# Kernel tuning notes

Hardware: AMD Instinct MI355X
Metric: run time of the kernel (lower is better)

Reference implementation:

```python
import jax, jax.numpy as jnp
import numpy as np

HID = 128
N_NODES = 50000
N_EDGES = 640000
N_GRAPHS = 64
N_LAYERS = 3
LN_EPS = 1e-5


def _ln(h, g, b):
    mu = jnp.mean(h, axis=-1, keepdims=True)
    v = jnp.mean(jnp.square(h - mu), axis=-1, keepdims=True)
    return (h - mu) * jax.lax.rsqrt(v + LN_EPS) * g + b


def _mlp2(h, W1, b1, g, be, W2, b2):
    # Linear -> ReLU -> LayerNorm -> (Dropout=identity in eval) -> Linear
    h = _ln(jax.nn.relu(h @ W1.T + b1), g, be)
    return h @ W2.T + b2


def _forward(x, edge_index, batch, axis_W1, axis_b1, axis_g, axis_be, axis_W2, axis_b2, org_W1, org_b1, org_g, org_be, org_W2, org_b2, nin_W, nin_b, conv_W1, conv_b1, conv_g, conv_be, conv_W2, conv_b2, eps, ln_g, ln_b, gate_W1, gate_b1, gate_g, gate_be, gate_W2, gate_b2, head_W1, head_b1, head_g, head_be, head_W2, head_b2):
    axis = x[:, 9:12]
    origin = x[:, 12:15]
    others = jnp.concatenate([x[:, :9], x[:, 15:19]], axis=1)  # [N, 13]
    axis_z = _mlp2(axis, axis_W1, axis_b1, axis_g, axis_be, axis_W2, axis_b2)
    org_z = _mlp2(origin, org_W1, org_b1, org_g, org_be, org_W2, org_b2)
    h = jnp.concatenate([others, axis_z, org_z], axis=1) @ nin_W.T + nin_b  # [N, HID]
    src, dst = edge_index[0], edge_index[1]
    n = x.shape[0]
    for l in range(N_LAYERS):
        res = h
        # GIN: sum-aggregate source features into targets (gather + scatter-add)
        agg = jax.ops.segment_sum(h[src], dst, num_segments=n)
        m = (1.0 + eps[l]) * h + agg
        m = _mlp2(m, conv_W1[l], conv_b1[l], conv_g[l], conv_be[l], conv_W2[l], conv_b2[l])
        h = _ln(jax.nn.relu(m), ln_g[l], ln_b[l]) + res
    # AttentionalAggregation: segment softmax over per-graph node gates
    gate = _mlp2(h, gate_W1, gate_b1, gate_g, gate_be, gate_W2, gate_b2)  # [N, 1]
    gmax = jax.ops.segment_max(gate, batch, num_segments=N_GRAPHS)
    e = jnp.exp(gate - gmax[batch])
    denom = jax.ops.segment_sum(e, batch, num_segments=N_GRAPHS)
    attn = e / denom[batch]
    g = jax.ops.segment_sum(attn * h, batch, num_segments=N_GRAPHS)  # [B, HID]
    logit = _mlp2(g, head_W1, head_b1, head_g, head_be, head_W2, head_b2)[:, 0]
    return logit


def setup_inputs() -> dict:
    key = jax.random.key(0)
    ks = iter(jax.random.split(key, 64))
    nk = lambda: next(ks)
    lin = lambda o, i: jax.random.normal(nk(), (o, i), jnp.float32) / np.float32(np.sqrt(i))
    lin3 = lambda L, o, i: jnp.stack([lin(o, i) for _ in range(L)])
    z = lambda *s: jnp.zeros(s, jnp.float32)
    o = lambda *s: jnp.ones(s, jnp.float32)
    inp = {}
    inp['x'] = jax.random.normal(nk(), (N_NODES, 19), jnp.float32)
    inp['edge_index'] = jax.random.randint(nk(), (2, N_EDGES), 0, N_NODES)
    inp['batch'] = jnp.sort(jax.random.randint(nk(), (N_NODES,), 0, N_GRAPHS))
    for p in ('axis', 'org'):
        inp[p + '_W1'] = lin(16, 3); inp[p + '_b1'] = z(16)
        inp[p + '_g'] = o(16); inp[p + '_be'] = z(16)
        inp[p + '_W2'] = lin(16, 16); inp[p + '_b2'] = z(16)
    inp['nin_W'] = lin(HID, 45); inp['nin_b'] = z(HID)
    inp['conv_W1'] = lin3(N_LAYERS, HID, HID); inp['conv_b1'] = z(N_LAYERS, HID)
    inp['conv_g'] = o(N_LAYERS, HID); inp['conv_be'] = z(N_LAYERS, HID)
    inp['conv_W2'] = lin3(N_LAYERS, HID, HID); inp['conv_b2'] = z(N_LAYERS, HID)
    inp['eps'] = z(N_LAYERS)
    inp['ln_g'] = o(N_LAYERS, HID); inp['ln_b'] = z(N_LAYERS, HID)
    for p in ('gate', 'head'):
        inp[p + '_W1'] = lin(HID // 2, HID); inp[p + '_b1'] = z(HID // 2)
        inp[p + '_g'] = o(HID // 2); inp[p + '_be'] = z(HID // 2)
        inp[p + '_W2'] = lin(1, HID // 2); inp[p + '_b2'] = z(1)
    return inp


def reference(x, edge_index, batch, axis_W1, axis_b1, axis_g, axis_be, axis_W2, axis_b2, org_W1, org_b1, org_g, org_be, org_W2, org_b2, nin_W, nin_b, conv_W1, conv_b1, conv_g, conv_be, conv_W2, conv_b2, eps, ln_g, ln_b, gate_W1, gate_b1, gate_g, gate_be, gate_W2, gate_b2, head_W1, head_b1, head_g, head_be, head_W2, head_b2):
    return _forward(x, edge_index, batch, axis_W1, axis_b1, axis_g, axis_be, axis_W2, axis_b2, org_W1, org_b1, org_g, org_be, org_W2, org_b2, nin_W, nin_b, conv_W1, conv_b1, conv_g, conv_be, conv_W2, conv_b2, eps, ln_g, ln_b, gate_W1, gate_b1, gate_g, gate_be, gate_W2, gate_b2, head_W1, head_b1, head_g, head_be, head_W2, head_b2)
```

## Files before the change

kernel.cpp:

```cpp
#include <hip/hip_runtime.h>

#define N_NODESC 50000
#define N_EDGESC 640000
#define N_GRAPHSC 64
#define HIDC 128
#define LN_EPSF 1e-5f
#define NGRID64 ((N_NODESC + 63) / 64)
#define PREP_ELEMS (8192 + 49152 + 49152)
#define WPREP_NB ((PREP_ELEMS + 255) / 256)
#define B1C 200
#define BCHUNK 3200
#define NBUK 98
#define WBUK 512

typedef short bf16x8 __attribute__((ext_vector_type(8)));
typedef float f32x4 __attribute__((ext_vector_type(4)));

static __device__ __forceinline__ unsigned short f2bf(float x) {
  unsigned u = __float_as_uint(x);
  u += 0x7fffu + ((u >> 16) & 1u);
  return (unsigned short)(u >> 16);
}
static __device__ __forceinline__ float bf2f(unsigned short b) {
  return __uint_as_float(((unsigned)b) << 16);
}

static __device__ __forceinline__ void mlp16(float in0, float in1, float in2,
    const float* __restrict__ W1, const float* __restrict__ b1,
    const float* __restrict__ g, const float* __restrict__ be,
    const float* __restrict__ W2, const float* __restrict__ b2,
    float* __restrict__ out) {
  float h[16];
  float s1 = 0.f, s2 = 0.f;
#pragma unroll
  for (int j = 0; j < 16; ++j) {
    float v = b1[j] + W1[j*3+0]*in0 + W1[j*3+1]*in1 + W1[j*3+2]*in2;
    v = fmaxf(v, 0.f);
    h[j] = v; s1 += v; s2 += v*v;
  }
  float mu = s1 * (1.f/16.f);
  float var = fmaxf(s2 * (1.f/16.f) - mu*mu, 0.f);
  float rs = rsqrtf(var + LN_EPSF);
  float z[16];
#pragma unroll
  for (int j = 0; j < 16; ++j) z[j] = (h[j]-mu)*rs*g[j] + be[j];
#pragma unroll
  for (int j = 0; j < 16; ++j) {
    float v = b2[j];
#pragma unroll
    for (int k = 0; k < 16; ++k) v += W2[j*16+k]*z[k];
    out[j] = v;
  }
}

__global__ __launch_bounds__(256) void bin_count_kernel(const int* __restrict__ ei,
    int* __restrict__ counts,
    float* __restrict__ Szero,
    const float* __restrict__ ninW, unsigned short* __restrict__ ninWb,
    const float* __restrict__ cW1, unsigned short* __restrict__ cW1b,
    const float* __restrict__ cW2, unsigned short* __restrict__ cW2b) {
  const int b = blockIdx.x;
  if (b < B1C) {
    __shared__ int cnt[NBUK];
    for (int i = threadIdx.x; i < NBUK; i += 256) cnt[i] = 0;
    __syncthreads();
    const int e0 = b * BCHUNK;
    const int e1 = e0 + BCHUNK;
    for (int e = e0 + threadIdx.x; e < e1; e += 256)
      atomicAdd(&cnt[ei[N_EDGESC + e] >> 9], 1);
    __syncthreads();
    for (int i = threadIdx.x; i < NBUK; i += 256)
      counts[i * B1C + b] = cnt[i];
  } else if (b == B1C) {
    for (int i = threadIdx.x; i < N_GRAPHSC * HIDC + N_GRAPHSC; i += 256)
      Szero[i] = 0.f;
  } else {
    int i = (b - B1C - 1) * 256 + threadIdx.x;
    if (i < 8192) {
      int f = i >> 6, k = i & 63;
      ninWb[i] = (k < 45) ? f2bf(ninW[f*45 + k]) : (unsigned short)0;
    } else if (i < 8192 + 49152) {
      int j = i - 8192;
      cW1b[j] = f2bf(cW1[j]);
    } else if (i < PREP_ELEMS) {
      int j = i - 8192 - 49152;
      cW2b[j] = f2bf(cW2[j]);
    }
  }
}

// ... 191 lines not shown
    int n = __shfl_up(c, off);
    if (lane >= off) c += n;
  }
  if (lane == 63) wsum[w] = c;
  __syncthreads();
  if (t == 0) {
    int run = 0;
#pragma unroll
    for (int k = 0; k < 4; ++k) { int x = wsum[k]; wsum[k] = run; run += x; }
  }
  __syncthreads();
  const int e1 = tot0 + c + wsum[w] - v1;
  hist[t] = e0;
  hist[256 + t] = e1;
  const int n0 = node0 + t, n1 = node0 + 256 + t;
  if (n0 < N_NODESC) rowptr[n0] = base + e0;
  if (n1 < N_NODESC) rowptr[n1] = base + e1;
  __syncthreads();
  for (int p = base + t; p < end; p += 256) {
    int2 pr = pairs[p];
    int slot = base + atomicAdd(&hist[pr.y - node0], 1);
    esrc[slot] = pr.x;
  }
  if (b == NBUK - 1 && t == 0) rowptr[N_NODESC] = N_EDGESC;
}

__global__ __launch_bounds__(128) void agg_kernel(const unsigned short* __restrict__ Hb,
    const int* __restrict__ rowptr, const int* __restrict__ esrc,
    const float* __restrict__ epsp, unsigned short* __restrict__ Mb) {
  const int t = threadIdx.x;
  const int c8 = t & 15;
  const int v  = t >> 4;
  const int node = blockIdx.x * 8 + v;
  if (node >= N_NODESC) return;
  const float e1 = 1.0f + epsp[0];
  bf16x8 h = *(const bf16x8*)&Hb[node*HIDC + c8*8];
  float acc[8];
#pragma unroll
  for (int k = 0; k < 8; ++k) acc[k] = 0.f;
  int s = rowptr[node];
  const int e = rowptr[node+1];
  for (; s + 8 <= e; s += 8) {
    int i0 = esrc[s],   i1 = esrc[s+1], i2 = esrc[s+2], i3 = esrc[s+3];
    int i4 = esrc[s+4], i5 = esrc[s+5], i6 = esrc[s+6], i7 = esrc[s+7];
    bf16x8 x0 = *(const bf16x8*)&Hb[i0*HIDC + c8*8];
    bf16x8 x1 = *(const bf16x8*)&Hb[i1*HIDC + c8*8];
    bf16x8 x2 = *(const bf16x8*)&Hb[i2*HIDC + c8*8];
    bf16x8 x3 = *(const bf16x8*)&Hb[i3*HIDC + c8*8];
    bf16x8 x4 = *(const bf16x8*)&Hb[i4*HIDC + c8*8];
    bf16x8 x5 = *(const bf16x8*)&Hb[i5*HIDC + c8*8];
    bf16x8 x6 = *(const bf16x8*)&Hb[i6*HIDC + c8*8];
    bf16x8 x7 = *(const bf16x8*)&Hb[i7*HIDC + c8*8];
#pragma unroll
    for (int k = 0; k < 8; ++k)
      acc[k] += ((bf2f((unsigned short)x0[k]) + bf2f((unsigned short)x1[k]))
               + (bf2f((unsigned short)x2[k]) + bf2f((unsigned short)x3[k])))
              + ((bf2f((unsigned short)x4[k]) + bf2f((unsigned short)x5[k]))
               + (bf2f((unsigned short)x6[k]) + bf2f((unsigned short)x7[k])));
  }
  for (; s + 4 <= e; s += 4) {
    int i0 = esrc[s], i1 = esrc[s+1], i2 = esrc[s+2], i3 = esrc[s+3];
    bf16x8 x0 = *(const bf16x8*)&Hb[i0*HIDC + c8*8];
    bf16x8 x1 = *(const bf16x8*)&Hb[i1*HIDC + c8*8];
    bf16x8 x2 = *(const bf16x8*)&Hb[i2*HIDC + c8*8];
    bf16x8 x3 = *(const bf16x8*)&Hb[i3*HIDC + c8*8];
#pragma unroll
    for (int k = 0; k < 8; ++k)
      acc[k] += (bf2f((unsigned short)x0[k]) + bf2f((unsigned short)x1[k]))
              + (bf2f((unsigned short)x2[k]) + bf2f((unsigned short)x3[k]));
  }
  for (; s < e; ++s) {
    bf16x8 x0 = *(const bf16x8*)&Hb[esrc[s]*HIDC + c8*8];
#pragma unroll
    for (int k = 0; k < 8; ++k) acc[k] += bf2f((unsigned short)x0[k]);
  }
  bf16x8 m8;
#pragma unroll
  for (int k = 0; k < 8; ++k)
    m8[k] = (short)f2bf(e1*bf2f((unsigned short)h[k]) + acc[k]);
  *(bf16x8*)&Mb[node*HIDC + c8*8] = m8;
}

template<bool GATE>
__global__ __launch_bounds__(256, 3) void gemmpair_kernel(
    const unsigned short* __restrict__ Mb,
    const unsigned short* __restrict__ Hin,
    const unsigned short* __restrict__ W1b, const float* __restrict__ b1,
    const float* __restrict__ g1, const float* __restrict__ be1,
    const unsigned short* __restrict__ W2b, const float* __restrict__ b2,
    const float* __restrict__ lng, const float* __restrict__ lnb,
    unsigned short* __restrict__ Hout,
    const float* __restrict__ gW1, const float* __restrict__ gb1,
    const float* __restrict__ glng, const float* __restrict__ glnb,
    const float* __restrict__ gW2, const float* __restrict__ gb2,
    const int* __restrict__ batch, float* __restrict__ S,
    float* __restrict__ denom) {
  __shared__ unsigned short Ab[64*136];
  __shared__ unsigned short Wl[128*136];
  __shared__ float Egate[64];
  __shared__ int   Sbatch[64];
  const int t = threadIdx.x;
  const int nb = blockIdx.x * 64;

#pragma unroll
  for (int i = 0; i < 4; ++i) {
    int chunk = t + i*256;
    int n = chunk >> 4, c8 = chunk & 15;
    int gn = nb + n;
    bf16x8 v = {0,0,0,0,0,0,0,0};
    if (gn < N_NODESC) v = *(const bf16x8*)&Mb[gn*HIDC + c8*8];
    *(bf16x8*)&Ab[n*136 + c8*8] = v;
  }
#pragma unroll
  for (int i = 0; i < 8; ++i) {
    int q = t + i*256;
    int f = q >> 4, c8 = q & 15;
    *(bf16x8*)&Wl[f*136 + c8*8] = *(const bf16x8*)&W1b[f*HIDC + c8*8];
  }
  __syncthreads();

  const int lane = t & 63, wv = t >> 6;
  const int quad = lane >> 4, l16 = lane & 15;
  const int arow = (wv*16 + l16)*136 + quad*8;

  f32x4 acc[8];
#pragma unroll
  for (int ft = 0; ft < 8; ++ft) acc[ft] = (f32x4){0.f,0.f,0.f,0.f};
#pragma unroll
  for (int ks = 0; ks < 4; ++ks) {
    bf16x8 a = *(const bf16x8*)(const void*)&Ab[arow + ks*32];
#pragma unroll
    for (int ft = 0; ft < 8; ++ft) {
      bf16x8 b = *(const bf16x8*)(const void*)&Wl[(ft*16 + l16)*136 + quad*8 + ks*32];
      acc[ft] = __builtin_amdgcn_mfma_f32_16x16x32_bf16(a, b, acc[ft], 0, 0, 0);
    }
  }

  {
    float bbv[8], gg[8], bee[8];
#pragma unroll
    for (int ft = 0; ft < 8; ++ft) {
      int f = ft*16 + l16;
      bbv[ft] = b1[f]; gg[ft] = g1[f]; bee[ft] = be1[f];
    }
    float s1[4] = {0,0,0,0}, s2[4] = {0,0,0,0};
#pragma unroll
    for (int ft = 0; ft < 8; ++ft)
#pragma unroll
      for (int r = 0; r < 4; ++r) {
        float v = fmaxf(acc[ft][r] + bbv[ft], 0.f);
        acc[ft][r] = v; s1[r] += v; s2[r] += v*v;
      }
#pragma unroll
    for (int m = 1; m < 16; m <<= 1)
#pragma unroll
      for (int r = 0; r < 4; ++r) {
        s1[r] += __shfl_xor(s1[r], m);
        s2[r] += __shfl_xor(s2[r], m);
      }
    float mu[4], rs[4];
#pragma unroll
    for (int r = 0; r < 4; ++r) {
      mu[r] = s1[r] * (1.f/128.f);
      float var = fmaxf(s2[r] * (1.f/128.f) - mu[r]*mu[r], 0.f);
      rs[r] = rsqrtf(var + LN_EPSF);
    }
    __syncthreads();
#pragma unroll
    for (int r = 0; r < 4; ++r) {
      int nloc = wv*16 + quad*4 + r;
#pragma unroll
      for (int ft = 0; ft < 8; ++ft) {
        float o = (acc[ft][r] - mu[r])*rs[r]*gg[ft] + bee[ft];
        Ab[nloc*136 + ft*16 + l16] = f2bf(o);
      }
    }
  }
#pragma unroll
  for (int i = 0; i < 8; ++i) {
    int q = t + i*256;
    int f = q >> 4, c8 = q & 15;
    *(bf16x8*)&Wl[f*136 + c8*8] = *(const bf16x8*)&W2b[f*HIDC + c8*8];
  }
  __syncthreads();

#pragma unroll
  for (int ft = 0; ft < 8; ++ft) acc[ft] = (f32x4){0.f,0.f,0.f,0.f};
#pragma unroll
  for (int ks = 0; ks < 4; ++ks) {
    bf16x8 a = *(const bf16x8*)(const void*)&Ab[arow + ks*32];
#pragma unroll
    for (int ft = 0; ft < 8; ++ft) {
      bf16x8 b = *(const bf16x8*)(const void*)&Wl[(ft*16 + l16)*136 + quad*8 + ks*32];
      acc[ft] = __builtin_amdgcn_mfma_f32_16x16x32_bf16(a, b, acc[ft], 0, 0, 0);
    }
  }

  {
    float bbv[8], gg[8], bee[8];
#pragma unroll
    for (int ft = 0; ft < 8; ++ft) {
      int f = ft*16 + l16;
      bbv[ft] = b2[f]; gg[ft] = lng[f]; bee[ft] = lnb[f];
    }
    float s1[4] = {0,0,0,0}, s2[4] = {0,0,0,0};
#pragma unroll
    for (int ft = 0; ft < 8; ++ft)
#pragma unroll
      for (int r = 0; r < 4; ++r) {
        float v = fmaxf(acc[ft][r] + bbv[ft], 0.f);
        acc[ft][r] = v; s1[r] += v; s2[r] += v*v;
      }
#pragma unroll
    for (int m = 1; m < 16; m <<= 1)
#pragma unroll
      for (int r = 0; r < 4; ++r) {
        s1[r] += __shfl_xor(s1[r], m);
        s2[r] += __shfl_xor(s2[r], m);
      }
    float mu[4], rs[4];
#pragma unroll
    for (int r = 0; r < 4; ++r) {
      mu[r] = s1[r] * (1.f/128.f);
      float var = fmaxf(s2[r] * (1.f/128.f) - mu[r]*mu[r], 0.f);
      rs[r] = rsqrtf(var + LN_EPSF);
    }
    __syncthreads();
#pragma unroll
    for (int r = 0; r < 4; ++r) {
      int nloc = wv*16 + quad*4 + r;
#pragma unroll
      for (int ft = 0; ft < 8; ++ft) {
        float o = (acc[ft][r] - mu[r])*rs[r]*gg[ft] + bee[ft];
        Ab[nloc*136 + ft*16 + l16] = f2bf(o);
      }
    }
  }
  __syncthreads();
#pragma unroll
  for (int i = 0; i < 4; ++i) {
    int chunk = t + i*256;
    int n = chunk >> 4, cc = chunk & 15;
    int gn = nb + n;
    bf16x8 o8 = {0,0,0,0,0,0,0,0};
    if (gn < N_NODESC) {
      bf16x8 vv = *(const bf16x8*)&Ab[n*136 + cc*8];
      bf16x8 rr = *(const bf16x8*)&Hin[gn*HIDC + cc*8];
#pragma unroll
      for (int k = 0; k < 8; ++k)
        o8[k] = (short)f2bf(bf2f((unsigned short)vv[k]) + bf2f((unsigned short)rr[k]));
      *(bf16x8*)&Hout[gn*HIDC + cc*8] = o8;
    }
    if (GATE) *(bf16x8*)&Ab[n*136 + cc*8] = o8;
  }

  if (GATE) {
#pragma unroll
    for (int i = 0; i < 8; ++i) {
      int q = t + i*256;
      int f = q >> 5, c4 = q & 31;
      float4 v = *(const float4*)&gW1[f*HIDC + c4*4];
      ushort4 hh;
      hh.x = f2bf(v.x); hh.y = f2bf(v.y); hh.z = f2bf(v.z); hh.w = f2bf(v.w);
      *(ushort4*)&Wl[f*136 + c4*4] = hh;
    }
    __syncthreads();

    f32x4 gacc[4];
#pragma unroll
    for (int ft = 0; ft < 4; ++ft) gacc[ft] = (f32x4){0.f,0.f,0.f,0.f};
#pragma unroll
    for (int ks = 0; ks < 4; ++ks) {
      bf16x8 a = *(const bf16x8*)(const void*)&Ab[arow + ks*32];
#pragma unroll
      for (int ft = 0; ft < 4; ++ft) {
        bf16x8 b = *(const bf16x8*)(const void*)&Wl[(ft*16 + l16)*136 + quad*8 + ks*32];
        gacc[ft] = __builtin_amdgcn_mfma_f32_16x16x32_bf16(a, b, gacc[ft], 0, 0, 0);
      }
    }

    float bbv[4], gg[4], bee[4], w2v[4];
#pragma unroll
    for (int ft = 0; ft < 4; ++ft) {
      int f = ft*16 + l16;
      bbv[ft] = gb1[f]; gg[ft] = glng[f]; bee[ft] = glnb[f]; w2v[ft] = gW2[f];
    }
    float s1[4] = {0,0,0,0}, s2[4] = {0,0,0,0};
#pragma unroll
    for (int ft = 0; ft < 4; ++ft)
#pragma unroll
      for (int r = 0; r < 4; ++r) {
        float v = fmaxf(gacc[ft][r] + bbv[ft], 0.f);
        gacc[ft][r] = v; s1[r] += v; s2[r] += v*v;
      }
#pragma unroll
    for (int m = 1; m < 16; m <<= 1)
#pragma unroll
      for (int r = 0; r < 4; ++r) {
        s1[r] += __shfl_xor(s1[r], m);
        s2[r] += __shfl_xor(s2[r], m);
      }
    float pd[4];
#pragma unroll
    for (int r = 0; r < 4; ++r) {
      float mu = s1[r] * (1.f/64.f);
      float var = fmaxf(s2[r] * (1.f/64.f) - mu*mu, 0.f);
      float rs = rsqrtf(var + LN_EPSF);
      float p = 0.f;
#pragma unroll
      for (int ft = 0; ft < 4; ++ft)
        p += ((gacc[ft][r] - mu)*rs*gg[ft] + bee[ft]) * w2v[ft];
      pd[r] = p;
    }
#pragma unroll
    for (int m = 1; m < 16; m <<= 1)
#pragma unroll
      for (int r = 0; r < 4; ++r) pd[r] += __shfl_xor(pd[r], m);
    if (l16 == 0) {
      float b2v = gb2[0];
#pragma unroll
      for (int r = 0; r < 4; ++r) {
        int nloc = wv*16 + quad*4 + r;
        int node = nb + nloc;
        if (node < N_NODESC) {
          Egate[nloc]  = expf(pd[r] + b2v);
          Sbatch[nloc] = batch[node];
        } else {
          Egate[nloc]  = 0.f;
          Sbatch[nloc] = -1;
        }
      }
    }
    __syncthreads();

    if (t < HIDC) {
      const int f = t;
      float accS = 0.f;
      int curG = Sbatch[0];
#pragma unroll 4
      for (int n = 0; n < 64; ++n) {
        int g = Sbatch[n];
        if (g != curG) {
          if (curG >= 0) atomicAdd(&S[curG*HIDC + f], accS);
          accS = 0.f; curG = g;
        }
        if (g >= 0) accS += Egate[n] * bf2f((unsigned short)Ab[n*136 + f]);
      }
      if (curG >= 0) atomicAdd(&S[curG*HIDC + f], accS);
    } else if (t == HIDC) {
      float accD = 0.f;
      int curG = Sbatch[0];
      for (int n = 0; n < 64; ++n) {
        int g = Sbatch[n];
        if (g != curG) {
          if (curG >= 0) atomicAdd(&denom[curG], accD);
          accD = 0.f; curG = g;
        }
        if (g >= 0) accD += Egate[n];
      }
      if (curG >= 0) atomicAdd(&denom[curG], accD);
    }
  }
}

__global__ __launch_bounds__(64) void head_kernel(const float* __restrict__ S,
    const float* __restrict__ denom, const float* __restrict__ W1,
    const float* __restrict__ b1, const float* __restrict__ g,
    const float* __restrict__ be, const float* __restrict__ W2,
    const float* __restrict__ b2, float* __restrict__ out) {
  const int gr = blockIdx.x;
  const int j = threadIdx.x;
  const float inv = 1.0f / denom[gr];
  float v = b1[j];
  for (int k = 0; k < HIDC; ++k) v += (S[gr*HIDC + k] * inv) * W1[j*HIDC + k];
  v = fmaxf(v, 0.f);
  float s1 = v, s2 = v*v;
  for (int off = 32; off; off >>= 1) { s1 += __shfl_xor(s1, off); s2 += __shfl_xor(s2, off); }
  float mu = s1 * (1.f/64.f);
  float var = fmaxf(s2 * (1.f/64.f) - mu*mu, 0.f);
  float rs = rsqrtf(var + LN_EPSF);
  float z = (v-mu)*rs*g[j] + be[j];
  float p = z * W2[j];
  for (int off = 32; off; off >>= 1) p += __shfl_xor(p, off);
  if (j == 0) out[gr] = p + b2[0];
}

extern "C" void kernel_launch(void* const* d_in, const int* in_sizes, int n_in,
                              void* d_out, int out_size, void* d_ws, size_t ws_size,
                              hipStream_t stream) {
  (void)in_sizes; (void)n_in; (void)out_size; (void)ws_size;
  const float* x     = (const float*)d_in[0];
  const int*   ei    = (const int*)d_in[1];
  const int*   batch = (const int*)d_in[2];
  const float* aW1 = (const float*)d_in[3];
  const float* ab1 = (const float*)d_in[4];
  const float* ag  = (const float*)d_in[5];
  const float* abe = (const float*)d_in[6];
  const float* aW2 = (const float*)d_in[7];
  const float* ab2 = (const float*)d_in[8];
  const float* oW1 = (const float*)d_in[9];
  const float* ob1 = (const float*)d_in[10];
  const float* og  = (const float*)d_in[11];
  const float* obe = (const float*)d_in[12];
  const float* oW2 = (const float*)d_in[13];
  const float* ob2 = (const float*)d_in[14];
  const float* ninW = (const float*)d_in[15];
  const float* ninb = (const float*)d_in[16];
  const float* cW1 = (const float*)d_in[17];
  const float* cb1 = (const float*)d_in[18];
  const float* cg  = (const float*)d_in[19];
  const float* cbe = (const float*)d_in[20];
  const float* cW2 = (const float*)d_in[21];
  const float* cb2 = (const float*)d_in[22];
  const float* eps = (const float*)d_in[23];
  const float* lng = (const float*)d_in[24];
  const float* lnb = (const float*)d_in[25];
  const float* gW1 = (const float*)d_in[26];
  const float* gb1 = (const float*)d_in[27];
  const float* gg  = (const float*)d_in[28];
  const float* gbe = (const float*)d_in[29];
  const float* gW2 = (const float*)d_in[30];
  const float* gb2 = (const float*)d_in[31];
  const float* hW1 = (const float*)d_in[32];
  const float* hb1 = (const float*)d_in[33];
  const float* hg  = (const float*)d_in[34];
  const float* hbe = (const float*)d_in[35];
  const float* hW2 = (const float*)d_in[36];
  const float* hb2 = (const float*)d_in[37];

  char* ws = (char*)d_ws;
  unsigned short* Ha = (unsigned short*)(ws + 0);
  unsigned short* Hc = (unsigned short*)(ws + 12800000);
  unsigned short* Mb = (unsigned short*)(ws + 25600000);
  int2* pairs  = (int2*)(ws + 25600000);
  int* counts  = (int*)(ws + 30720000);
  int* offl    = (int*)(ws + 30800000);
  int* btot    = (int*)(ws + 30880000);
  int* bb      = (int*)(ws + 30881024);
  float* S     = (float*)(ws + 38800000);
  float* denom = (float*)(ws + 38832768);
  int* rowptr  = (int*)(ws + 38833280);
  int* esrc    = (int*)(ws + 39233284);
  unsigned short* ninWb = (unsigned short*)(ws + 41800000);
  unsigned short* cW1b  = (unsigned short*)(ws + 41816384);
  unsigned short* cW2b  = (unsigned short*)(ws + 41914688);

  bin_count_kernel<<<B1C + 1 + WPREP_NB, 256, 0, stream>>>(
      ei, counts, S, ninW, ninWb, cW1, cW1b, cW2, cW2b);
  bin_scanA_kernel<<<NBUK, 256, 0, stream>>>(counts, offl, btot);
  bin_scanB_kernel<<<1, 128, 0, stream>>>(btot, bb);
  bin_write_enc_kernel<<<B1C + NGRID64, 256, 0, stream>>>(
      ei, offl, bb, pairs,
      x, aW1, ab1, ag, abe, aW2, ab2,
      oW1, ob1, og, obe, oW2, ob2,
      ninWb, ninb, Ha);
  bucket_build_kernel<<<NBUK, 256, 0, stream>>>(pairs, bb, rowptr, esrc);

  unsigned short* cur = Ha;
  unsigned short* nxt = Hc;
  for (int l = 0; l < 3; ++l) {
    agg_kernel<<<(N_NODESC + 7) / 8, 128, 0, stream>>>(cur, rowptr, esrc, eps + l, Mb);
    if (l < 2) {
      gemmpair_kernel<false><<<NGRID64, 256, 0, stream>>>(
          Mb, cur,
          cW1b + l*HIDC*HIDC, cb1 + l*HIDC, cg + l*HIDC, cbe + l*HIDC,
          cW2b + l*HIDC*HIDC, cb2 + l*HIDC, lng + l*HIDC, lnb + l*HIDC,
          nxt,
          gW1, gb1, gg, gbe, gW2, gb2, batch, S, denom);
    } else {
      gemmpair_kernel<true><<<NGRID64, 256, 0, stream>>>(
          Mb, cur,
          cW1b + l*HIDC*HIDC, cb1 + l*HIDC, cg + l*HIDC, cbe + l*HIDC,
          cW2b + l*HIDC*HIDC, cb2 + l*HIDC, lng + l*HIDC, lnb + l*HIDC,
          nxt,
          gW1, gb1, gg, gbe, gW2, gb2, batch, S, denom);
    }
    unsigned short* tmp = cur; cur = nxt; nxt = tmp;
  }

  head_kernel<<<N_GRAPHSC, 64, 0, stream>>>(S, denom, hW1, hb1, hg, hbe, hW2, hb2,
                                            (float*)d_out);
}
```

Before: 327.7 us.

## Make gemmpair kernel persistent with resident weights and prefetched tiles

```diff
diff --git a/kernel.cpp b/kernel.cpp
--- a/kernel.cpp
+++ b/kernel.cpp
@@ -6,6 +6,7 @@
 #define HIDC 128
 #define LN_EPSF 1e-5f
 #define NGRID64 ((N_NODESC + 63) / 64)
+#define GPGRID 256
 #define PREP_ELEMS (8192 + 49152 + 49152)
 #define WPREP_NB ((PREP_ELEMS + 255) / 256)
 #define B1C 200
@@ -363,7 +364,7 @@
 }
 
 template<bool GATE>
-__global__ __launch_bounds__(256, 3) void gemmpair_kernel(
+__global__ __launch_bounds__(256, 1) void gemmpair_kernel(
     const unsigned short* __restrict__ Mb,
     const unsigned short* __restrict__ Hin,
     const unsigned short* __restrict__ W1b, const float* __restrict__ b1,
@@ -376,165 +377,24 @@
     const float* __restrict__ gW2, const float* __restrict__ gb2,
     const int* __restrict__ batch, float* __restrict__ S,
     float* __restrict__ denom) {
-  __shared__ unsigned short Ab[64*136];
-  __shared__ unsigned short Wl[128*136];
+  __shared__ unsigned short W1l[128*136];
+  __shared__ unsigned short W2l[128*136];
+  __shared__ unsigned short Wgl[64*136];
+  __shared__ unsigned short Ab[2][64*136];
   __shared__ float Egate[64];
   __shared__ int   Sbatch[64];
   const int t = threadIdx.x;
-  const int nb = blockIdx.x * 64;
-
-#pragma unroll
-  for (int i = 0; i < 4; ++i) {
-    int chunk = t + i*256;
-    int n = chunk >> 4, c8 = chunk & 15;
-    int gn = nb + n;
-    bf16x8 v = {0,0,0,0,0,0,0,0};
-    if (gn < N_NODESC) v = *(const bf16x8*)&Mb[gn*HIDC + c8*8];
-    *(bf16x8*)&Ab[n*136 + c8*8] = v;
-  }
+  const int lane = t & 63, wv = t >> 6;
+  const int quad = lane >> 4, l16 = lane & 15;
+  const int arow0 = (wv*16 + l16)*136 + quad*8;
+
 #pragma unroll
   for (int i = 0; i < 8; ++i) {
     int q = t + i*256;
     int f = q >> 4, c8 = q & 15;
-    *(bf16x8*)&Wl[f*136 + c8*8] = *(const bf16x8*)&W1b[f*HIDC + c8*8];
-  }
-  __syncthreads();
-
-  const int lane = t & 63, wv = t >> 6;
-  const int quad = lane >> 4, l16 = lane & 15;
-  const int arow = (wv*16 + l16)*136 + quad*8;
-
-  f32x4 acc[8];
-#pragma unroll
-  for (int ft = 0; ft < 8; ++ft) acc[ft] = (f32x4){0.f,0.f,0.f,0.f};
-#pragma unroll
-  for (int ks = 0; ks < 4; ++ks) {
-    bf16x8 a = *(const bf16x8*)(const void*)&Ab[arow + ks*32];
-#pragma unroll
-    for (int ft = 0; ft < 8; ++ft) {
-      bf16x8 b = *(const bf16x8*)(const void*)&Wl[(ft*16 + l16)*136 + quad*8 + ks*32];
-      acc[ft] = __builtin_amdgcn_mfma_f32_16x16x32_bf16(a, b, acc[ft], 0, 0, 0);
-    }
-  }
-
-  {
-    float bbv[8], gg[8], bee[8];
-#pragma unroll
-    for (int ft = 0; ft < 8; ++ft) {
-      int f = ft*16 + l16;
-      bbv[ft] = b1[f]; gg[ft] = g1[f]; bee[ft] = be1[f];
-    }
-    float s1[4] = {0,0,0,0}, s2[4] = {0,0,0,0};
-#pragma unroll
-    for (int ft = 0; ft < 8; ++ft)
-#pragma unroll
-      for (int r = 0; r < 4; ++r) {
-        float v = fmaxf(acc[ft][r] + bbv[ft], 0.f);
-        acc[ft][r] = v; s1[r] += v; s2[r] += v*v;
-      }
-#pragma unroll
-    for (int m = 1; m < 16; m <<= 1)
-#pragma unroll
-      for (int r = 0; r < 4; ++r) {
-        s1[r] += __shfl_xor(s1[r], m);
-        s2[r] += __shfl_xor(s2[r], m);
-      }
-    float mu[4], rs[4];
-#pragma unroll
-    for (int r = 0; r < 4; ++r) {
-      mu[r] = s1[r] * (1.f/128.f);
-      float var = fmaxf(s2[r] * (1.f/128.f) - mu[r]*mu[r], 0.f);
-      rs[r] = rsqrtf(var + LN_EPSF);
-    }
-    __syncthreads();
-#pragma unroll
-    for (int r = 0; r < 4; ++r) {
-      int nloc = wv*16 + quad*4 + r;
-#pragma unroll
-      for (int ft = 0; ft < 8; ++ft) {
-        float o = (acc[ft][r] - mu[r])*rs[r]*gg[ft] + bee[ft];
-        Ab[nloc*136 + ft*16 + l16] = f2bf(o);
-      }
-    }
-  }
-#pragma unroll
-  for (int i = 0; i < 8; ++i) {
-    int q = t + i*256;
-    int f = q >> 4, c8 = q & 15;
-    *(bf16x8*)&Wl[f*136 + c8*8] = *(const bf16x8*)&W2b[f*HIDC + c8*8];
-  }
-  __syncthreads();
-
-#pragma unroll
-  for (int ft = 0; ft < 8; ++ft) acc[ft] = (f32x4){0.f,0.f,0.f,0.f};
-#pragma unroll
-  for (int ks = 0; ks < 4; ++ks) {
-    bf16x8 a = *(const bf16x8*)(const void*)&Ab[arow + ks*32];
-#pragma unroll
-    for (int ft = 0; ft < 8; ++ft) {
-      bf16x8 b = *(const bf16x8*)(const void*)&Wl[(ft*16 + l16)*136 + quad*8 + ks*32];
-      acc[ft] = __builtin_amdgcn_mfma_f32_16x16x32_bf16(a, b, acc[ft], 0, 0, 0);
-    }
-  }
-
-  {
-    float bbv[8], gg[8], bee[8];
-#pragma unroll
-    for (int ft = 0; ft < 8; ++ft) {
-      int f = ft*16 + l16;
-      bbv[ft] = b2[f]; gg[ft] = lng[f]; bee[ft] = lnb[f];
-    }
-    float s1[4] = {0,0,0,0}, s2[4] = {0,0,0,0};
-#pragma unroll
-    for (int ft = 0; ft < 8; ++ft)
-#pragma unroll
-      for (int r = 0; r < 4; ++r) {
-        float v = fmaxf(acc[ft][r] + bbv[ft], 0.f);
-        acc[ft][r] = v; s1[r] += v; s2[r] += v*v;
-      }
-#pragma unroll
-    for (int m = 1; m < 16; m <<= 1)
-#pragma unroll
-      for (int r = 0; r < 4; ++r) {
-        s1[r] += __shfl_xor(s1[r], m);
-        s2[r] += __shfl_xor(s2[r], m);
-      }
-    float mu[4], rs[4];
-#pragma unroll
-    for (int r = 0; r < 4; ++r) {
-      mu[r] = s1[r] * (1.f/128.f);
-      float var = fmaxf(s2[r] * (1.f/128.f) - mu[r]*mu[r], 0.f);
-      rs[r] = rsqrtf(var + LN_EPSF);
-    }
-    __syncthreads();
-#pragma unroll
-    for (int r = 0; r < 4; ++r) {
-      int nloc = wv*16 + quad*4 + r;
-#pragma unroll
-      for (int ft = 0; ft < 8; ++ft) {
-        float o = (acc[ft][r] - mu[r])*rs[r]*gg[ft] + bee[ft];
-        Ab[nloc*136 + ft*16 + l16] = f2bf(o);
-      }
-    }
-  }
-  __syncthreads();
-#pragma unroll
-  for (int i = 0; i < 4; ++i) {
-    int chunk = t + i*256;
-    int n = chunk >> 4, cc = chunk & 15;
-    int gn = nb + n;
-    bf16x8 o8 = {0,0,0,0,0,0,0,0};
-    if (gn < N_NODESC) {
-      bf16x8 vv = *(const bf16x8*)&Ab[n*136 + cc*8];
-      bf16x8 rr = *(const bf16x8*)&Hin[gn*HIDC + cc*8];
-#pragma unroll
-      for (int k = 0; k < 8; ++k)
-        o8[k] = (short)f2bf(bf2f((unsigned short)vv[k]) + bf2f((unsigned short)rr[k]));
-      *(bf16x8*)&Hout[gn*HIDC + cc*8] = o8;
-    }
-    if (GATE) *(bf16x8*)&Ab[n*136 + cc*8] = o8;
-  }
-
+    *(bf16x8*)&W1l[f*136 + c8*8] = *(const bf16x8*)&W1b[f*HIDC + c8*8];
+    *(bf16x8*)&W2l[f*136 + c8*8] = *(const bf16x8*)&W2b[f*HIDC + c8*8];
+  }
   if (GATE) {
 #pragma unroll
     for (int i = 0; i < 8; ++i) {
@@ -543,104 +403,279 @@
       float4 v = *(const float4*)&gW1[f*HIDC + c4*4];
       ushort4 hh;
       hh.x = f2bf(v.x); hh.y = f2bf(v.y); hh.z = f2bf(v.z); hh.w = f2bf(v.w);
-      *(ushort4*)&Wl[f*136 + c4*4] = hh;
+      *(ushort4*)&Wgl[f*136 + c4*4] = hh;
+    }
+  }
+
+  int tile = blockIdx.x;
+  bf16x8 pM[4], pH[4];
+#pragma unroll
+  for (int i = 0; i < 4; ++i) {
+    int chunk = t + i*256;
+    int n = chunk >> 4, c8 = chunk & 15;
+    int gn = tile*64 + n;
+    bf16x8 vM = {0,0,0,0,0,0,0,0}, vH = {0,0,0,0,0,0,0,0};
+    if (tile < NGRID64 && gn < N_NODESC) {
+      vM = *(const bf16x8*)&Mb[gn*HIDC + c8*8];
+      vH = *(const bf16x8*)&Hin[gn*HIDC + c8*8];
+    }
+    pM[i] = vM; pH[i] = vH;
+  }
+
+  int cur = 0;
+  for (; tile < NGRID64; tile += GPGRID) {
+    const int nb = tile * 64;
+#pragma unroll
+    for (int i = 0; i < 4; ++i) {
+      int chunk = t + i*256;
+      int n = chunk >> 4, c8 = chunk & 15;
+      *(bf16x8*)&Ab[cur][n*136 + c8*8] = pM[i];
     }
     __syncthreads();
 
-    f32x4 gacc[4];
-#pragma unroll
-    for (int ft = 0; ft < 4; ++ft) gacc[ft] = (f32x4){0.f,0.f,0.f,0.f};
+    bf16x8 nM[4], nH[4];
+    const int ntile = tile + GPGRID;
+#pragma unroll
+    for (int i = 0; i < 4; ++i) {
+      int chunk = t + i*256;
+      int n = chunk >> 4, c8 = chunk & 15;
+      int gn = ntile*64 + n;
+      bf16x8 vM = {0,0,0,0,0,0,0,0}, vH = {0,0,0,0,0,0,0,0};
+      if (ntile < NGRID64 && gn < N_NODESC) {
+        vM = *(const bf16x8*)&Mb[gn*HIDC + c8*8];
+        vH = *(const bf16x8*)&Hin[gn*HIDC + c8*8];
+      }
+      nM[i] = vM; nH[i] = vH;
+    }
+
+    f32x4 acc[8];
+#pragma unroll
+    for (int ft = 0; ft < 8; ++ft) acc[ft] = (f32x4){0.f,0.f,0.f,0.f};
 #pragma unroll
     for (int ks = 0; ks < 4; ++ks) {
-      bf16x8 a = *(const bf16x8*)(const void*)&Ab[arow + ks*32];
-#pragma unroll
-      for (int ft = 0; ft < 4; ++ft) {
-        bf16x8 b = *(const bf16x8*)(const void*)&Wl[(ft*16 + l16)*136 + quad*8 + ks*32];
-        gacc[ft] = __builtin_amdgcn_mfma_f32_16x16x32_bf16(a, b, gacc[ft], 0, 0, 0);
-      }
-    }
-
-    float bbv[4], gg[4], bee[4], w2v[4];
-#pragma unroll
-    for (int ft = 0; ft < 4; ++ft) {
-      int f = ft*16 + l16;
-      bbv[ft] = gb1[f]; gg[ft] = glng[f]; bee[ft] = glnb[f]; w2v[ft] = gW2[f];
-    }
-    float s1[4] = {0,0,0,0}, s2[4] = {0,0,0,0};
-#pragma unroll
-    for (int ft = 0; ft < 4; ++ft)
+      bf16x8 a = *(const bf16x8*)(const void*)&Ab[cur][arow0 + ks*32];
+#pragma unroll
+      for (int ft = 0; ft < 8; ++ft) {
+        bf16x8 b = *(const bf16x8*)(const void*)&W1l[(ft*16 + l16)*136 + quad*8 + ks*32];
+        acc[ft] = __builtin_amdgcn_mfma_f32_16x16x32_bf16(a, b, acc[ft], 0, 0, 0);
+      }
+    }
+
+    {
+      float bbv[8], gg[8], bee[8];
+#pragma unroll
+      for (int ft = 0; ft < 8; ++ft) {
+        int f = ft*16 + l16;
+        bbv[ft] = b1[f]; gg[ft] = g1[f]; bee[ft] = be1[f];
+      }
+      float s1[4] = {0,0,0,0}, s2[4] = {0,0,0,0};
+#pragma unroll
+      for (int ft = 0; ft < 8; ++ft)
+#pragma unroll
+        for (int r = 0; r < 4; ++r) {
+          float v = fmaxf(acc[ft][r] + bbv[ft], 0.f);
+          acc[ft][r] = v; s1[r] += v; s2[r] += v*v;
+        }
+#pragma unroll
+      for (int m = 1; m < 16; m <<= 1)
+#pragma unroll
+        for (int r = 0; r < 4; ++r) {
+          s1[r] += __shfl_xor(s1[r], m);
+          s2[r] += __shfl_xor(s2[r], m);
+        }
+      float mu[4], rs[4];
 #pragma unroll
       for (int r = 0; r < 4; ++r) {
-        float v = fmaxf(gacc[ft][r] + bbv[ft], 0.f);
-        gacc[ft][r] = v; s1[r] += v; s2[r] += v*v;
-      }
-#pragma unroll
-    for (int m = 1; m < 16; m <<= 1)
-#pragma unroll
-      for (int r = 0; r < 4; ++r) {
-        s1[r] += __shfl_xor(s1[r], m);
-        s2[r] += __shfl_xor(s2[r], m);
-      }
-    float pd[4];
-#pragma unroll
-    for (int r = 0; r < 4; ++r) {
-      float mu = s1[r] * (1.f/64.f);
-      float var = fmaxf(s2[r] * (1.f/64.f) - mu*mu, 0.f);
-      float rs = rsqrtf(var + LN_EPSF);
-      float p = 0.f;
-#pragma unroll
-      for (int ft = 0; ft < 4; ++ft)
-        p += ((gacc[ft][r] - mu)*rs*gg[ft] + bee[ft]) * w2v[ft];
-      pd[r] = p;
-    }
-#pragma unroll
-    for (int m = 1; m < 16; m <<= 1)
-#pragma unroll
-      for (int r = 0; r < 4; ++r) pd[r] += __shfl_xor(pd[r], m);
-    if (l16 == 0) {
-      float b2v = gb2[0];
+        mu[r] = s1[r] * (1.f/128.f);
+        float var = fmaxf(s2[r] * (1.f/128.f) - mu[r]*mu[r], 0.f);
+        rs[r] = rsqrtf(var + LN_EPSF);
+      }
+      __syncthreads();
 #pragma unroll
       for (int r = 0; r < 4; ++r) {
         int nloc = wv*16 + quad*4 + r;
-        int node = nb + nloc;
-        if (node < N_NODESC) {
-          Egate[nloc]  = expf(pd[r] + b2v);
-          Sbatch[nloc] = batch[node];
-        } else {
-          Egate[nloc]  = 0.f;
-          Sbatch[nloc] = -1;
+#pragma unroll
+        for (int ft = 0; ft < 8; ++ft) {
+          float o = (acc[ft][r] - mu[r])*rs[r]*gg[ft] + bee[ft];
+          Ab[cur][nloc*136 + ft*16 + l16] = f2bf(o);
         }
       }
     }
     __syncthreads();
 
-    if (t < HIDC) {
-      const int f = t;
-      float accS = 0.f;
-      int curG = Sbatch[0];
+#pragma unroll
+    for (int ft = 0; ft < 8; ++ft) acc[ft] = (f32x4){0.f,0.f,0.f,0.f};
+#pragma unroll
+    for (int ks = 0; ks < 4; ++ks) {
+      bf16x8 a = *(const bf16x8*)(const void*)&Ab[cur][arow0 + ks*32];
+#pragma unroll
+      for (int ft = 0; ft < 8; ++ft) {
+        bf16x8 b = *(const bf16x8*)(const void*)&W2l[(ft*16 + l16)*136 + quad*8 + ks*32];
+        acc[ft] = __builtin_amdgcn_mfma_f32_16x16x32_bf16(a, b, acc[ft], 0, 0, 0);
+      }
+    }
+
+    {
+      float bbv[8], gg[8], bee[8];
+#pragma unroll
+      for (int ft = 0; ft < 8; ++ft) {
+        int f = ft*16 + l16;
+        bbv[ft] = b2[f]; gg[ft] = lng[f]; bee[ft] = lnb[f];
+      }
+      float s1[4] = {0,0,0,0}, s2[4] = {0,0,0,0};
+#pragma unroll
+      for (int ft = 0; ft < 8; ++ft)
+#pragma unroll
+        for (int r = 0; r < 4; ++r) {
+          float v = fmaxf(acc[ft][r] + bbv[ft], 0.f);
+          acc[ft][r] = v; s1[r] += v; s2[r] += v*v;
+        }
+#pragma unroll
+      for (int m = 1; m < 16; m <<= 1)
+#pragma unroll
+        for (int r = 0; r < 4; ++r) {
+          s1[r] += __shfl_xor(s1[r], m);
+          s2[r] += __shfl_xor(s2[r], m);
+        }
+      float mu[4], rs[4];
+#pragma unroll
+      for (int r = 0; r < 4; ++r) {
+        mu[r] = s1[r] * (1.f/128.f);
+        float var = fmaxf(s2[r] * (1.f/128.f) - mu[r]*mu[r], 0.f);
+        rs[r] = rsqrtf(var + LN_EPSF);
+      }
+      __syncthreads();
+#pragma unroll
+      for (int r = 0; r < 4; ++r) {
+        int nloc = wv*16 + quad*4 + r;
+#pragma unroll
+        for (int ft = 0; ft < 8; ++ft) {
+          float o = (acc[ft][r] - mu[r])*rs[r]*gg[ft] + bee[ft];
+          Ab[cur][nloc*136 + ft*16 + l16] = f2bf(o);
+        }
+      }
+    }
+    __syncthreads();
+
+#pragma unroll
+    for (int i = 0; i < 4; ++i) {
+      int chunk = t + i*256;
+      int n = chunk >> 4, cc = chunk & 15;
+      int gn = nb + n;
+      bf16x8 o8 = {0,0,0,0,0,0,0,0};
+      if (gn < N_NODESC) {
+        bf16x8 vv = *(const bf16x8*)&Ab[cur][n*136 + cc*8];
+        bf16x8 rr = pH[i];
+#pragma unroll
+        for (int k = 0; k < 8; ++k)
+          o8[k] = (short)f2bf(bf2f((unsigned short)vv[k]) + bf2f((unsigned short)rr[k]));
+        *(bf16x8*)&Hout[gn*HIDC + cc*8] = o8;
+      }
+      if (GATE) *(bf16x8*)&Ab[cur][n*136 + cc*8] = o8;
+    }
+
+    if (GATE) {
+      __syncthreads();
+
+      f32x4 gacc[4];
+#pragma unroll
+      for (int ft = 0; ft < 4; ++ft) gacc[ft] = (f32x4){0.f,0.f,0.f,0.f};
+#pragma unroll
+      for (int ks = 0; ks < 4; ++ks) {
+        bf16x8 a = *(const bf16x8*)(const void*)&Ab[cur][arow0 + ks*32];
+#pragma unroll
+        for (int ft = 0; ft < 4; ++ft) {
+          bf16x8 b = *(const bf16x8*)(const void*)&Wgl[(ft*16 + l16)*136 + quad*8 + ks*32];
+          gacc[ft] = __builtin_amdgcn_mfma_f32_16x16x32_bf16(a, b, gacc[ft], 0, 0, 0);
+        }
+      }
+
+      float bbv[4], gg[4], bee[4], w2v[4];
+#pragma unroll
+      for (int ft = 0; ft < 4; ++ft) {
+        int f = ft*16 + l16;
+        bbv[ft] = gb1[f]; gg[ft] = glng[f]; bee[ft] = glnb[f]; w2v[ft] = gW2[f];
+      }
+      float s1[4] = {0,0,0,0}, s2[4] = {0,0,0,0};
+#pragma unroll
+      for (int ft = 0; ft < 4; ++ft)
+#pragma unroll
+        for (int r = 0; r < 4; ++r) {
+          float v = fmaxf(gacc[ft][r] + bbv[ft], 0.f);
+          gacc[ft][r] = v; s1[r] += v; s2[r] += v*v;
+        }
+#pragma unroll
+      for (int m = 1; m < 16; m <<= 1)
+#pragma unroll
+        for (int r = 0; r < 4; ++r) {
+          s1[r] += __shfl_xor(s1[r], m);
+          s2[r] += __shfl_xor(s2[r], m);
+        }
+      float pd[4];
+#pragma unroll
+      for (int r = 0; r < 4; ++r) {
+        float mu = s1[r] * (1.f/64.f);
+        float var = fmaxf(s2[r] * (1.f/64.f) - mu*mu, 0.f);
+        float rs = rsqrtf(var + LN_EPSF);
+        float p = 0.f;
+#pragma unroll
+        for (int ft = 0; ft < 4; ++ft)
+          p += ((gacc[ft][r] - mu)*rs*gg[ft] + bee[ft]) * w2v[ft];
+        pd[r] = p;
+      }
+#pragma unroll
+      for (int m = 1; m < 16; m <<= 1)
+#pragma unroll
+        for (int r = 0; r < 4; ++r) pd[r] += __shfl_xor(pd[r], m);
+      if (l16 == 0) {
+        float b2v = gb2[0];
+#pragma unroll
+        for (int r = 0; r < 4; ++r) {
+          int nloc = wv*16 + quad*4 + r;
+          int node = nb + nloc;
+          if (node < N_NODESC) {
+            Egate[nloc]  = expf(pd[r] + b2v);
+            Sbatch[nloc] = batch[node];
+          } else {
+            Egate[nloc]  = 0.f;
+            Sbatch[nloc] = -1;
+          }
+        }
+      }
+      __syncthreads();
+
+      if (t < HIDC) {
+        const int f = t;
+        float accS = 0.f;
+        int curG = Sbatch[0];
 #pragma unroll 4
-      for (int n = 0; n < 64; ++n) {
-        int g = Sbatch[n];
-        if (g != curG) {
-          if (curG >= 0) atomicAdd(&S[curG*HIDC + f], accS);
-          accS = 0.f; curG = g;
-        }
-        if (g >= 0) accS += Egate[n] * bf2f((unsigned short)Ab[n*136 + f]);
-      }
-      if (curG >= 0) atomicAdd(&S[curG*HIDC + f], accS);
-    } else if (t == HIDC) {
-      float accD = 0.f;
-      int curG = Sbatch[0];
-      for (int n = 0; n < 64; ++n) {
-        int g = Sbatch[n];
-        if (g != curG) {
-          if (curG >= 0) atomicAdd(&denom[curG], accD);
-          accD = 0.f; curG = g;
-        }
-        if (g >= 0) accD += Egate[n];
-      }
-      if (curG >= 0) atomicAdd(&denom[curG], accD);
-    }
+        for (int n = 0; n < 64; ++n) {
+          int g = Sbatch[n];
+          if (g != curG) {
+            if (curG >= 0) atomicAdd(&S[curG*HIDC + f], accS);
+            accS = 0.f; curG = g;
+          }
+          if (g >= 0) accS += Egate[n] * bf2f((unsigned short)Ab[cur][n*136 + f]);
+        }
+        if (curG >= 0) atomicAdd(&S[curG*HIDC + f], accS);
+      } else if (t == HIDC) {
+        float accD = 0.f;
+        int curG = Sbatch[0];
+        for (int n = 0; n < 64; ++n) {
+          int g = Sbatch[n];
+          if (g != curG) {
+            if (curG >= 0) atomicAdd(&denom[curG], accD);
+            accD = 0.f; curG = g;
+          }
+          if (g >= 0) accD += Egate[n];
+        }
+        if (curG >= 0) atomicAdd(&denom[curG], accD);
+      }
+    }
+
+#pragma unroll
+    for (int i = 0; i < 4; ++i) { pM[i] = nM[i]; pH[i] = nH[i]; }
+    cur ^= 1;
   }
 }
 
@@ -742,14 +777,14 @@
   for (int l = 0; l < 3; ++l) {
     agg_kernel<<<(N_NODESC + 7) / 8, 128, 0, stream>>>(cur, rowptr, esrc, eps + l, Mb);
     if (l < 2) {
-      gemmpair_kernel<false><<<NGRID64, 256, 0, stream>>>(
+      gemmpair_kernel<false><<<GPGRID, 256, 0, stream>>>(
           Mb, cur,
           cW1b + l*HIDC*HIDC, cb1 + l*HIDC, cg + l*HIDC, cbe + l*HIDC,
           cW2b + l*HIDC*HIDC, cb2 + l*HIDC, lng + l*HIDC, lnb + l*HIDC,
           nxt,
           gW1, gb1, gg, gbe, gW2, gb2, batch, S, denom);
     } else {
-      gemmpair_kernel<true><<<NGRID64, 256, 0, stream>>>(
+      gemmpair_kernel<true><<<GPGRID, 256, 0, stream>>>(
           Mb, cur,
           cW1b + l*HIDC*HIDC, cb1 + l*HIDC, cg + l*HIDC, cbe + l*HIDC,
           cW2b + l*HIDC*HIDC, cb2 + l*HIDC, lng + l*HIDC, lnb + l*HIDC,
```

New measurement: 358.3 us. 9.3% more time.

## Make gemmpair per-wavefront independent with weights read directly from global memory

Applied to the files above, without the earlier changes.

```diff
diff --git a/kernel.cpp b/kernel.cpp
--- a/kernel.cpp
+++ b/kernel.cpp
@@ -6,6 +6,8 @@
 #define HIDC 128
 #define LN_EPSF 1e-5f
 #define NGRID64 ((N_NODESC + 63) / 64)
+#define NT16 (N_NODESC / 16)
+#define GPGRID ((NT16 + 3) / 4)
 #define PREP_ELEMS (8192 + 49152 + 49152)
 #define WPREP_NB ((PREP_ELEMS + 255) / 256)
 #define B1C 200
@@ -363,7 +365,7 @@
 }
 
 template<bool GATE>
-__global__ __launch_bounds__(256, 3) void gemmpair_kernel(
+__global__ __launch_bounds__(256, 2) void gemmpair_kernel(
     const unsigned short* __restrict__ Mb,
     const unsigned short* __restrict__ Hin,
     const unsigned short* __restrict__ W1b, const float* __restrict__ b1,
@@ -376,45 +378,39 @@
     const float* __restrict__ gW2, const float* __restrict__ gb2,
     const int* __restrict__ batch, float* __restrict__ S,
     float* __restrict__ denom) {
-  __shared__ unsigned short Ab[64*136];
-  __shared__ unsigned short Wl[128*136];
-  __shared__ float Egate[64];
-  __shared__ int   Sbatch[64];
+  __shared__ unsigned short Tl[4][16*136 + 8];
+  __shared__ float EgL[4][16];
+  __shared__ int   GbL[4][16];
   const int t = threadIdx.x;
-  const int nb = blockIdx.x * 64;
-
+  const int wv = t >> 6, lane = t & 63;
+  const int quad = lane >> 4, l16 = lane & 15;
+  const int wtile = blockIdx.x * 4 + wv;
+  if (wtile >= NT16) return;
+  const int nb = wtile * 16;
+  unsigned short* Tw = Tl[wv];
+
+  f32x4 acc[8];
+#pragma unroll
+  for (int ft = 0; ft < 8; ++ft) acc[ft] = (f32x4){0.f,0.f,0.f,0.f};
+  {
+    const unsigned short* Arow = &Mb[(nb + l16)*HIDC + quad*8];
+#pragma unroll
+    for (int ks = 0; ks < 4; ++ks) {
+      bf16x8 a = *(const bf16x8*)&Arow[ks*32];
+#pragma unroll
+      for (int ft = 0; ft < 8; ++ft) {
+        bf16x8 b = *(const bf16x8*)&W1b[(ft*16 + l16)*HIDC + quad*8 + ks*32];
+        acc[ft] = __builtin_amdgcn_mfma_f32_16x16x32_bf16(a, b, acc[ft], 0, 0, 0);
+      }
+    }
+  }
+
+  bf16x8 pH[4];
 #pragma unroll
   for (int i = 0; i < 4; ++i) {
-    int chunk = t + i*256;
+    int chunk = lane + i*64;
     int n = chunk >> 4, c8 = chunk & 15;
-    int gn = nb + n;
-    bf16x8 v = {0,0,0,0,0,0,0,0};
-    if (gn < N_NODESC) v = *(const bf16x8*)&Mb[gn*HIDC + c8*8];
-    *(bf16x8*)&Ab[n*136 + c8*8] = v;
-  }
-#pragma unroll
-  for (int i = 0; i < 8; ++i) {
-    int q = t + i*256;
-    int f = q >> 4, c8 = q & 15;
-    *(bf16x8*)&Wl[f*136 + c8*8] = *(const bf16x8*)&W1b[f*HIDC + c8*8];
-  }
-  __syncthreads();
-
-  const int lane = t & 63, wv = t >> 6;
-  const int quad = lane >> 4, l16 = lane & 15;
-  const int arow = (wv*16 + l16)*136 + quad*8;
-
-  f32x4 acc[8];
-#pragma unroll
-  for (int ft = 0; ft < 8; ++ft) acc[ft] = (f32x4){0.f,0.f,0.f,0.f};
-#pragma unroll
-  for (int ks = 0; ks < 4; ++ks) {
-    bf16x8 a = *(const bf16x8*)(const void*)&Ab[arow + ks*32];
-#pragma unroll
-    for (int ft = 0; ft < 8; ++ft) {
-      bf16x8 b = *(const bf16x8*)(const void*)&Wl[(ft*16 + l16)*136 + quad*8 + ks*32];
-      acc[ft] = __builtin_amdgcn_mfma_f32_16x16x32_bf16(a, b, acc[ft], 0, 0, 0);
-    }
+    pH[i] = *(const bf16x8*)&Hin[(nb + n)*HIDC + c8*8];
   }
 
   {
@@ -439,40 +435,28 @@
         s1[r] += __shfl_xor(s1[r], m);
         s2[r] += __shfl_xor(s2[r], m);
       }
-    float mu[4], rs[4];
 #pragma unroll
     for (int r = 0; r < 4; ++r) {
-      mu[r] = s1[r] * (1.f/128.f);
-      float var = fmaxf(s2[r] * (1.f/128.f) - mu[r]*mu[r], 0.f);
-      rs[r] = rsqrtf(var + LN_EPSF);
-    }
-    __syncthreads();
-#pragma unroll
-    for (int r = 0; r < 4; ++r) {
-      int nloc = wv*16 + quad*4 + r;
+      float mu = s1[r] * (1.f/128.f);
+      float var = fmaxf(s2[r] * (1.f/128.f) - mu*mu, 0.f);
+      float rs = rsqrtf(var + LN_EPSF);
+      int nloc = quad*4 + r;
 #pragma unroll
       for (int ft = 0; ft < 8; ++ft) {
-        float o = (acc[ft][r] - mu[r])*rs[r]*gg[ft] + bee[ft];
-        Ab[nloc*136 + ft*16 + l16] = f2bf(o);
-      }
-    }
-  }
-#pragma unroll
-  for (int i = 0; i < 8; ++i) {
-    int q = t + i*256;
-    int f = q >> 4, c8 = q & 15;
-    *(bf16x8*)&Wl[f*136 + c8*8] = *(const bf16x8*)&W2b[f*HIDC + c8*8];
-  }
-  __syncthreads();
+        float o = (acc[ft][r] - mu)*rs*gg[ft] + bee[ft];
+        Tw[nloc*136 + ft*16 + l16] = f2bf(o);
+      }
+    }
+  }
 
 #pragma unroll
   for (int ft = 0; ft < 8; ++ft) acc[ft] = (f32x4){0.f,0.f,0.f,0.f};
 #pragma unroll
   for (int ks = 0; ks < 4; ++ks) {
-    bf16x8 a = *(const bf16x8*)(const void*)&Ab[arow + ks*32];
+    bf16x8 a = *(const bf16x8*)(const void*)&Tw[l16*136 + quad*8 + ks*32];
 #pragma unroll
     for (int ft = 0; ft < 8; ++ft) {
-      bf16x8 b = *(const bf16x8*)(const void*)&Wl[(ft*16 + l16)*136 + quad*8 + ks*32];
+      bf16x8 b = *(const bf16x8*)&W2b[(ft*16 + l16)*HIDC + quad*8 + ks*32];
       acc[ft] = __builtin_amdgcn_mfma_f32_16x16x32_bf16(a, b, acc[ft], 0, 0, 0);
     }
   }
@@ -499,64 +483,53 @@
         s1[r] += __shfl_xor(s1[r], m);
         s2[r] += __shfl_xor(s2[r], m);
       }
-    float mu[4], rs[4];
 #pragma unroll
     for (int r = 0; r < 4; ++r) {
-      mu[r] = s1[r] * (1.f/128.f);
-      float var = fmaxf(s2[r] * (1.f/128.f) - mu[r]*mu[r], 0.f);
-      rs[r] = rsqrtf(var + LN_EPSF);
-    }
-    __syncthreads();
-#pragma unroll
-    for (int r = 0; r < 4; ++r) {
-      int nloc = wv*16 + quad*4 + r;
+      float mu = s1[r] * (1.f/128.f);
+      float var = fmaxf(s2[r] * (1.f/128.f) - mu*mu, 0.f);
+      float rs = rsqrtf(var + LN_EPSF);
+      int nloc = quad*4 + r;
 #pragma unroll
       for (int ft = 0; ft < 8; ++ft) {
-        float o = (acc[ft][r] - mu[r])*rs[r]*gg[ft] + bee[ft];
-        Ab[nloc*136 + ft*16 + l16] = f2bf(o);
-      }
-    }
-  }
-  __syncthreads();
+        float o = (acc[ft][r] - mu)*rs*gg[ft] + bee[ft];
+        Tw[nloc*136 + ft*16 + l16] = f2bf(o);
+      }
+    }
+  }
+
 #pragma unroll
   for (int i = 0; i < 4; ++i) {
-    int chunk = t + i*256;
+    int chunk = lane + i*64;
     int n = chunk >> 4, cc = chunk & 15;
     int gn = nb + n;
-    bf16x8 o8 = {0,0,0,0,0,0,0,0};
-    if (gn < N_NODESC) {
-      bf16x8 vv = *(const bf16x8*)&Ab[n*136 + cc*8];
-      bf16x8 rr = *(const bf16x8*)&Hin[gn*HIDC + cc*8];
-#pragma unroll
-      for (int k = 0; k < 8; ++k)
-        o8[k] = (short)f2bf(bf2f((unsigned short)vv[k]) + bf2f((unsigned short)rr[k]));
-      *(bf16x8*)&Hout[gn*HIDC + cc*8] = o8;
-    }
-    if (GATE) *(bf16x8*)&Ab[n*136 + cc*8] = o8;
+    bf16x8 vv = *(const bf16x8*)&Tw[n*136 + cc*8];
+    bf16x8 rr = pH[i];
+    bf16x8 o8;
+#pragma unroll
+    for (int k = 0; k < 8; ++k)
+      o8[k] = (short)f2bf(bf2f((unsigned short)vv[k]) + bf2f((unsigned short)rr[k]));
+    *(bf16x8*)&Hout[gn*HIDC + cc*8] = o8;
+    if (GATE) *(bf16x8*)&Tw[n*136 + cc*8] = o8;
   }
 
   if (GATE) {
-#pragma unroll
-    for (int i = 0; i < 8; ++i) {
-      int q = t + i*256;
-      int f = q >> 5, c4 = q & 31;
-      float4 v = *(const float4*)&gW1[f*HIDC + c4*4];
-      ushort4 hh;
-      hh.x = f2bf(v.x); hh.y = f2bf(v.y); hh.z = f2bf(v.z); hh.w = f2bf(v.w);
-      *(ushort4*)&Wl[f*136 + c4*4] = hh;
-    }
-    __syncthreads();
-
     f32x4 gacc[4];
 #pragma unroll
     for (int ft = 0; ft < 4; ++ft) gacc[ft] = (f32x4){0.f,0.f,0.f,0.f};
 #pragma unroll
     for (int ks = 0; ks < 4; ++ks) {
-      bf16x8 a = *(const bf16x8*)(const void*)&Ab[arow + ks*32];
+      bf16x8 a = *(const bf16x8*)(const void*)&Tw[l16*136 + quad*8 + ks*32];
 #pragma unroll
       for (int ft = 0; ft < 4; ++ft) {
-        bf16x8 b = *(const bf16x8*)(const void*)&Wl[(ft*16 + l16)*136 + quad*8 + ks*32];
-        gacc[ft] = __builtin_amdgcn_mfma_f32_16x16x32_bf16(a, b, gacc[ft], 0, 0, 0);
+        const float* wp = &gW1[(ft*16 + l16)*HIDC + quad*8 + ks*32];
+        float4 w0 = *(const float4*)wp;
+        float4 w1 = *(const float4*)(wp + 4);
+        bf16x8 wb;
+        wb[0] = (short)f2bf(w0.x); wb[1] = (short)f2bf(w0.y);
+        wb[2] = (short)f2bf(w0.z); wb[3] = (short)f2bf(w0.w);
+        wb[4] = (short)f2bf(w1.x); wb[5] = (short)f2bf(w1.y);
+        wb[6] = (short)f2bf(w1.z); wb[7] = (short)f2bf(w1.w);
+        gacc[ft] = __builtin_amdgcn_mfma_f32_16x16x32_bf16(a, wb, gacc[ft], 0, 0, 0);
       }
     }
 
@@ -601,45 +574,33 @@
       float b2v = gb2[0];
 #pragma unroll
       for (int r = 0; r < 4; ++r) {
-        int nloc = wv*16 + quad*4 + r;
-        int node = nb + nloc;
-        if (node < N_NODESC) {
-          Egate[nloc]  = expf(pd[r] + b2v);
-          Sbatch[nloc] = batch[node];
-        } else {
-          Egate[nloc]  = 0.f;
-          Sbatch[nloc] = -1;
+        int nloc = quad*4 + r;
+        EgL[wv][nloc] = expf(pd[r] + b2v);
+        GbL[wv][nloc] = batch[nb + nloc];
+      }
+    }
+
+    {
+      float a0 = 0.f, a1 = 0.f, aD = 0.f;
+      int curG = GbL[wv][0];
+#pragma unroll
+      for (int n = 0; n < 16; ++n) {
+        int g = GbL[wv][n];
+        float E = EgL[wv][n];
+        if (g != curG) {
+          atomicAdd(&S[curG*HIDC + 2*lane], a0);
+          atomicAdd(&S[curG*HIDC + 2*lane + 1], a1);
+          if (lane == 0) atomicAdd(&denom[curG], aD);
+          a0 = a1 = aD = 0.f; curG = g;
         }
-      }
-    }
-    __syncthreads();
-
-    if (t < HIDC) {
-      const int f = t;
-      float accS = 0.f;
-      int curG = Sbatch[0];
-#pragma unroll 4
-      for (int n = 0; n < 64; ++n) {
-        int g = Sbatch[n];
-        if (g != curG) {
-          if (curG >= 0) atomicAdd(&S[curG*HIDC + f], accS);
-          accS = 0.f; curG = g;
-        }
-        if (g >= 0) accS += Egate[n] * bf2f((unsigned short)Ab[n*136 + f]);
-      }
-      if (curG >= 0) atomicAdd(&S[curG*HIDC + f], accS);
-    } else if (t == HIDC) {
-      float accD = 0.f;
-      int curG = Sbatch[0];
-      for (int n = 0; n < 64; ++n) {
-        int g = Sbatch[n];
-        if (g != curG) {
-          if (curG >= 0) atomicAdd(&denom[curG], accD);
-          accD = 0.f; curG = g;
-        }
-        if (g >= 0) accD += Egate[n];
-      }
-      if (curG >= 0) atomicAdd(&denom[curG], accD);
+        unsigned pp = *(const unsigned*)&Tw[n*136 + 2*lane];
+        a0 += E * bf2f((unsigned short)(pp & 0xffffu));
+        a1 += E * bf2f((unsigned short)(pp >> 16));
+        aD += E;
+      }
+      atomicAdd(&S[curG*HIDC + 2*lane], a0);
+      atomicAdd(&S[curG*HIDC + 2*lane + 1], a1);
+      if (lane == 0) atomicAdd(&denom[curG], aD);
     }
   }
 }
@@ -742,14 +703,14 @@
   for (int l = 0; l < 3; ++l) {
     agg_kernel<<<(N_NODESC + 7) / 8, 128, 0, stream>>>(cur, rowptr, esrc, eps + l, Mb);
     if (l < 2) {
-      gemmpair_kernel<false><<<NGRID64, 256, 0, stream>>>(
+      gemmpair_kernel<false><<<GPGRID, 256, 0, stream>>>(
           Mb, cur,
           cW1b + l*HIDC*HIDC, cb1 + l*HIDC, cg + l*HIDC, cbe + l*HIDC,
           cW2b + l*HIDC*HIDC, cb2 + l*HIDC, lng + l*HIDC, lnb + l*HIDC,
           nxt,
           gW1, gb1, gg, gbe, gW2, gb2, batch, S, denom);
     } else {
-      gemmpair_kernel<true><<<NGRID64, 256, 0, stream>>>(
+      gemmpair_kernel<true><<<GPGRID, 256, 0, stream>>>(
           Mb, cur,
           cW1b + l*HIDC*HIDC, cb1 + l*HIDC, cg + l*HIDC, cbe + l*HIDC,
           cW2b + l*HIDC*HIDC, cb2 + l*HIDC, lng + l*HIDC, lnb + l*HIDC,
```

Result: slower. 390.1 us (+19.0%).
